# Kernel tuning notes

Measured on AMD Instinct MI355X. Metric: run time of the kernel, lower is better.

## Reference

```python
import jax, jax.numpy as jnp
import numpy as np

B, F_DIM, C, M = 16, 64, 64, 512
OUT_CH = 32
DT = 1.0


def setup_inputs() -> dict:
    key = jax.random.key(0)
    ks = jax.random.split(key, 8)
    x = jax.random.normal(ks[0], (B, F_DIM, C, M), dtype=jnp.float32)
    A = jax.random.uniform(ks[1], (B, M, C, C), dtype=jnp.float32)
    phys_prior = jax.random.normal(ks[2], (B, C, M), dtype=jnp.float32)
    kappa = jnp.array(0.1, dtype=jnp.float32)
    alpha = jnp.array(0.05, dtype=jnp.float32)
    # r_phi MLP: Linear(1,16) -> ELU -> Linear(16,1)
    w1 = jax.random.normal(ks[3], (16, 1), dtype=jnp.float32) * 1.0
    b1 = jnp.zeros((16,), dtype=jnp.float32)
    w2 = jax.random.normal(ks[4], (1, 16), dtype=jnp.float32) * 0.25
    b2 = jnp.zeros((1,), dtype=jnp.float32)
    # 1x1 Conv2d(1, OUT_CH): weight (OUT_CH,1,1,1) -> flatten to (OUT_CH,)
    pw = jax.random.normal(ks[5], (OUT_CH,), dtype=jnp.float32)
    pb = jnp.zeros((OUT_CH,), dtype=jnp.float32)
    return {"x": x, "A": A, "phys_prior": phys_prior, "kappa": kappa,
            "alpha": alpha, "w1": w1, "b1": b1, "w2": w2, "b2": b2,
            "pw": pw, "pb": pb}


def reference(x, A, phys_prior, kappa, alpha, w1, b1, w2, b2, pw, pb):
    # x: (B,F,C,M), A: (B,M,C,C), phys_prior: (B,C,M)
    s = x.mean(axis=1)                      # (B,C,M)
    deg = A.sum(axis=-1)                    # (B,M,C)
    sT = jnp.transpose(s, (0, 2, 1))        # (B,M,C)
    # torch einsum 'bmcd,bmcn->bmdn' with n=1 contracts over c: (A^T s)
    As = jnp.einsum('bmcd,bmc->bmd', A, sT)  # (B,M,C)
    Ls = jnp.transpose(deg * sT - As, (0, 2, 1))  # (B,C,M)
    k = jax.nn.softplus(kappa)
    # tiny MLP on per-(b,c) mean over M
    r_in = s.mean(axis=-1, keepdims=True)   # (B,C,1)
    h = jax.nn.elu(r_in @ w1.T + b1)        # (B,C,16)
    r = h @ w2.T + b2                       # (B,C,1), broadcasts over M
    phys_corr = alpha * phys_prior          # (B,C,M)
    s_new = s - DT * k * Ls + DT * (r + phys_corr)  # (B,C,M)
    # 1x1 conv over (B,1,C,M): pointwise scale+bias per output channel
    corr = s_new[:, None, :, :] * pw[None, :, None, None] + pb[None, :, None, None]
    return corr  # (B,OUT_CH,C,M)
```

## Files before the change

kernel.cpp:

```cpp
#include <hip/hip_runtime.h>
#include <math.h>

#define B_  16
#define F_  64
#define C_  64
#define M_  512
#define OC_ 32

typedef float vf4 __attribute__((ext_vector_type(4)));

__global__ __launch_bounds__(128, 6) void k1_mean(
    const float* __restrict__ x,
    float* __restrict__ s_out, float* __restrict__ rpart)
{
    const int gid = blockIdx.x;
    const int q   = gid & 3;
    const int bc  = gid >> 2;
    const int b   = bc >> 6;
    const int c   = bc & 63;
    const int t   = threadIdx.x;
    const int tf  = t >> 5;
    const int tm  = t & 31;
    const int m4  = (q << 5) + tm;

    const size_t rowbase = ((size_t)b * F_ * C_ + c) * M_;
    float ax = 0.f, ay = 0.f, az = 0.f, aw = 0.f;
    #pragma unroll 8
    for (int j = 0; j < 16; ++j) {
        const int f = (tf << 4) + j;
        const float4 v = ((const float4*)(x + rowbase + (size_t)f * C_ * M_))[m4];
        ax += v.x; ay += v.y; az += v.z; aw += v.w;
    }

    __shared__ float4 red[4][32];
    red[tf][tm] = make_float4(ax, ay, az, aw);
    __syncthreads();

    if (tf == 0) {
        const float4 r1 = red[1][tm], r2 = red[2][tm], r3 = red[3][tm];
        const float inv_f = 1.0f / (float)F_;
        float4 sv;
        sv.x = (ax + r1.x + r2.x + r3.x) * inv_f;
        sv.y = (ay + r1.y + r2.y + r3.y) * inv_f;
        sv.z = (az + r1.z + r2.z + r3.z) * inv_f;
        sv.w = (aw + r1.w + r2.w + r3.w) * inv_f;
        ((float4*)(s_out + (size_t)bc * M_))[m4] = sv;

        float p = sv.x + sv.y + sv.z + sv.w;
        #pragma unroll
        for (int off = 16; off > 0; off >>= 1) p += __shfl_xor(p, off);
        if (t == 0) rpart[gid] = p;
    }
}

__global__ __launch_bounds__(1024, 8) void k2_fused(
    const float* __restrict__ A, const float* __restrict__ phys,
    const float* __restrict__ kappa_p, const float* __restrict__ alpha_p,
    const float* __restrict__ s_in, const float* __restrict__ rpart,
    const float* __restrict__ w1, const float* __restrict__ b1,
    const float* __restrict__ w2, const float* __restrict__ b2,
    const float* __restrict__ pw, const float* __restrict__ pb,
    float* __restrict__ out)
{
    __shared__ float Ab[2][4096];
    __shared__ float sl[16 * 68];
    __shared__ float ph[16 * 68];
    __shared__ float snl[64 * 17];
    __shared__ float redA[16 * 64];
    __shared__ float degL[C_];

    const int t   = threadIdx.x;
    const int blk = blockIdx.x;
    const int b   = blk >> 5;
    const int m0  = (blk & 31) << 4;

    {
        const int cc = t >> 4;
        const int mi = t & 15;
        const size_t g = ((size_t)(b * C_ + cc)) * M_ + m0 + mi;
        sl[mi * 68 + cc] = s_in[g];
        ph[mi * 68 + cc] = phys[g];
    }

    float r_c = 0.f;
    if (t < 64) {
        const float4 rp = ((const float4*)rpart)[b * C_ + t];
        const float rin = (rp.x + rp.y + rp.z + rp.w) * (1.0f / (float)M_);
        r_c = b2[0];
        #pragma unroll
        for (int j = 0; j < 16; ++j) {
            float hh = rin * w1[j] + b1[j];
            hh = (hh > 0.f) ? hh : (expf(hh) - 1.f);
            r_c += hh * w2[j];
        }
    }

    const float* Abase = A + (size_t)(b * M_ + m0) * (C_ * C_);
    float4 v = ((const float4*)Abase)[t];
    ((float4*)Ab[0])[t] = v;
    __syncthreads();

    const float kcoef = log1pf(expf(kappa_p[0]));
    const float al    = alpha_p[0];
    const int c   = t & 63;
    const int g   = t >> 6;
    const int row = t >> 4;
    const int h   = t & 15;

    #pragma unroll 1
    for (int i = 0; i < 16; ++i) {
        const int cur = i & 1;

        float4 vn;
        if (i < 15)
            vn = ((const float4*)(Abase + (size_t)(i + 1) * (C_ * C_)))[t];

        float p = v.x + v.y + v.z + v.w;
        p += __shfl_xor(p, 1);
        p += __shfl_xor(p, 2);
        p += __shfl_xor(p, 4);
        p += __shfl_xor(p, 8);
        if (h == 0) degL[row] = p;

        const float s0 = sl[i * 68 + 4 * g + 0];
        const float s1 = sl[i * 68 + 4 * g + 1];
        const float s2 = sl[i * 68 + 4 * g + 2];
        const float s3 = sl[i * 68 + 4 * g + 3];
        const float ap = Ab[cur][(4 * g + 0) * 64 + c] * s0
                       + Ab[cur][(4 * g + 1) * 64 + c] * s1
                       + Ab[cur][(4 * g + 2) * 64 + c] * s2
                       + Ab[cur][(4 * g + 3) * 64 + c] * s3;
        redA[g * 64 + c] = ap;
        __syncthreads();

        if (t < 64) {
            float As = 0.f;
            #pragma unroll
            for (int gg = 0; gg < 16; ++gg) As += redA[gg * 64 + t];
            const float dg   = degL[t];
            const float sval = sl[i * 68 + t];
            const float pv   = ph[i * 68 + t];
            snl[t * 17 + i] = sval - kcoef * (dg * sval - As) + (r_c + al * pv);
        }
        if (i < 15) {
            ((float4*)Ab[cur ^ 1])[t] = vn;
            v = vn;
        }
        __syncthreads();
    }

    #pragma unroll
    for (int i = 0; i < 8; ++i) {
        const int idx = (i << 10) + t;
        const int mq  = idx & 3;
        const int cc  = (idx >> 2) & 63;
        const int o   = idx >> 8;
        const float w  = pw[o];
        const float bb = pb[o];
        vf4 ov;
        ov.x = snl[cc * 17 + mq * 4 + 0] * w + bb;
        ov.y = snl[cc * 17 + mq * 4 + 1] * w + bb;
        ov.z = snl[cc * 17 + mq * 4 + 2] * w + bb;
        ov.w = snl[cc * 17 + mq * 4 + 3] * w + bb;
        __builtin_nontemporal_store(ov,
            (vf4*)(out + (((size_t)(b * OC_ + o)) * C_ + cc) * M_ + m0 + mq * 4));
    }
}

extern "C" void kernel_launch(void* const* d_in, const int* in_sizes, int n_in,
                              void* d_out, int out_size, void* d_ws, size_t ws_size,
                              hipStream_t stream)
{
    const float* x     = (const float*)d_in[0];
    const float* A     = (const float*)d_in[1];
    const float* phys  = (const float*)d_in[2];
    const float* kappa = (const float*)d_in[3];
    const float* alpha = (const float*)d_in[4];
    const float* w1    = (const float*)d_in[5];
    const float* b1    = (const float*)d_in[6];
    const float* w2    = (const float*)d_in[7];
    const float* b2    = (const float*)d_in[8];
    const float* pw    = (const float*)d_in[9];
    const float* pb    = (const float*)d_in[10];
    float* out = (float*)d_out;

    float* ws    = (float*)d_ws;
    float* s     = ws;
    float* rpart = ws + (size_t)B_ * C_ * M_;

    k1_mean<<<B_ * C_ * 4, 128, 0, stream>>>(x, s, rpart);
    k2_fused<<<B_ * (M_ / 16), 1024, 0, stream>>>(A, phys, kappa, alpha, s, rpart,
                                                  w1, b1, w2, b2, pw, pb, out);
}
```

Before: 65.37 us.

## Deepen A prefetch to two slices ahead with double-buffered degree staging

Restructures the per-slice loop in the fused kernel so global loads of A run two slices ahead. Each slice's LDS staging and degree shuffle-reduction now overlap with the current slice's matvec. Degree values get a double buffer so staging the next slice does not clobber the current one. This aims to hide global-load latency better, at the cost of an extra register set of A values and the same number of barriers per slice.

Measured after the change: 65.47 us. No clear change (+0.1%).

```diff
diff --git a/kernel.cpp b/kernel.cpp
--- a/kernel.cpp
+++ b/kernel.cpp
@@ -67,7 +67,7 @@
     __shared__ float ph[16 * 68];
     __shared__ float snl[64 * 17];
     __shared__ float redA[16 * 64];
-    __shared__ float degL[C_];
+    __shared__ float degL[2][C_];
 
     const int t   = threadIdx.x;
     const int blk = blockIdx.x;
@@ -77,9 +77,9 @@
     {
         const int cc = t >> 4;
         const int mi = t & 15;
-        const size_t g = ((size_t)(b * C_ + cc)) * M_ + m0 + mi;
-        sl[mi * 68 + cc] = s_in[g];
-        ph[mi * 68 + cc] = phys[g];
+        const size_t gg = ((size_t)(b * C_ + cc)) * M_ + m0 + mi;
+        sl[mi * 68 + cc] = s_in[gg];
+        ph[mi * 68 + cc] = phys[gg];
     }
 
     float r_c = 0.f;
@@ -96,56 +96,72 @@
     }
 
     const float* Abase = A + (size_t)(b * M_ + m0) * (C_ * C_);
-    float4 v = ((const float4*)Abase)[t];
-    ((float4*)Ab[0])[t] = v;
-    __syncthreads();
-
-    const float kcoef = log1pf(expf(kappa_p[0]));
-    const float al    = alpha_p[0];
-    const int c   = t & 63;
-    const int g   = t >> 6;
-    const int row = t >> 4;
-    const int h   = t & 15;
-
-    #pragma unroll 1
-    for (int i = 0; i < 16; ++i) {
-        const int cur = i & 1;
-
-        float4 vn;
-        if (i < 15)
-            vn = ((const float4*)(Abase + (size_t)(i + 1) * (C_ * C_)))[t];
-
-        float p = v.x + v.y + v.z + v.w;
+    const int h    = t & 15;
+    const int rowi = t >> 4;
+    const int c    = t & 63;
+    const int g    = t >> 6;
+
+    auto stage_and_deg = [&](const float4& vv, int buf) {
+        ((float4*)Ab[buf])[t] = vv;
+        float p = vv.x + vv.y + vv.z + vv.w;
         p += __shfl_xor(p, 1);
         p += __shfl_xor(p, 2);
         p += __shfl_xor(p, 4);
         p += __shfl_xor(p, 8);
-        if (h == 0) degL[row] = p;
-
+        if (h == 0) degL[buf][rowi] = p;
+    };
+
+    auto compute = [&](int buf, int i) {
         const float s0 = sl[i * 68 + 4 * g + 0];
         const float s1 = sl[i * 68 + 4 * g + 1];
         const float s2 = sl[i * 68 + 4 * g + 2];
         const float s3 = sl[i * 68 + 4 * g + 3];
-        const float ap = Ab[cur][(4 * g + 0) * 64 + c] * s0
-                       + Ab[cur][(4 * g + 1) * 64 + c] * s1
-                       + Ab[cur][(4 * g + 2) * 64 + c] * s2
-                       + Ab[cur][(4 * g + 3) * 64 + c] * s3;
+        const float ap = Ab[buf][(4 * g + 0) * 64 + c] * s0
+                       + Ab[buf][(4 * g + 1) * 64 + c] * s1
+                       + Ab[buf][(4 * g + 2) * 64 + c] * s2
+                       + Ab[buf][(4 * g + 3) * 64 + c] * s3;
         redA[g * 64 + c] = ap;
-        __syncthreads();
-
+    };
+
+    const float kcoef = log1pf(expf(kappa_p[0]));
+    const float al    = alpha_p[0];
+
+    auto combine = [&](int buf, int i) {
         if (t < 64) {
             float As = 0.f;
             #pragma unroll
-            for (int gg = 0; gg < 16; ++gg) As += redA[gg * 64 + t];
-            const float dg   = degL[t];
+            for (int q2 = 0; q2 < 16; ++q2) As += redA[q2 * 64 + t];
+            const float dg   = degL[buf][t];
             const float sval = sl[i * 68 + t];
             const float pv   = ph[i * 68 + t];
             snl[t * 17 + i] = sval - kcoef * (dg * sval - As) + (r_c + al * pv);
         }
-        if (i < 15) {
-            ((float4*)Ab[cur ^ 1])[t] = vn;
-            v = vn;
-        }
+    };
+
+    float4 vA = ((const float4*)Abase)[t];
+    stage_and_deg(vA, 0);
+    float4 vB = ((const float4*)(Abase + 4096))[t];
+    __syncthreads();
+
+    #pragma unroll 1
+    for (int ii = 0; ii < 8; ++ii) {
+        const int i0 = 2 * ii;
+        if (i0 + 2 < 16)
+            vA = ((const float4*)(Abase + (size_t)(i0 + 2) * 4096))[t];
+        compute(0, i0);
+        stage_and_deg(vB, 1);
+        __syncthreads();
+        combine(0, i0);
+        __syncthreads();
+
+        const int i1 = i0 + 1;
+        if (i1 + 2 < 16)
+            vB = ((const float4*)(Abase + (size_t)(i1 + 2) * 4096))[t];
+        compute(1, i1);
+        if (i1 + 1 < 16)
+            stage_and_deg(vA, 0);
+        __syncthreads();
+        combine(1, i1);
         __syncthreads();
     }
 
```
